# Kernel tuning notes

Hardware: AMD Instinct MI355X
Metric: run time of the kernel (lower is better)

## Reference

```python
import jax, jax.numpy as jnp
import numpy as np

VOCAB, EMB_DIM, HIDDEN, NUM_CLASSES = 50000, 300, 1000, 5
B, MAX_LEN = 4096, 128


def setup_inputs() -> dict:
    key = jax.random.key(0)
    k1, k2, k3, k4, k5, k6, k7 = jax.random.split(key, 7)
    x = jax.random.randint(k1, (B, MAX_LEN), 0, VOCAB, dtype=jnp.int64)
    lengths = jnp.maximum(jax.random.randint(k2, (B,), 0, MAX_LEN, dtype=jnp.int64), 1)
    emb_table = jax.random.normal(k3, (VOCAB, EMB_DIM), dtype=jnp.float32) * 0.1
    W1 = jax.random.normal(k4, (2 * EMB_DIM, HIDDEN), dtype=jnp.float32) * (1.0 / np.sqrt(2 * EMB_DIM))
    b1 = jax.random.normal(k5, (HIDDEN,), dtype=jnp.float32) * 0.01
    W2 = jax.random.normal(k6, (HIDDEN, NUM_CLASSES), dtype=jnp.float32) * (1.0 / np.sqrt(HIDDEN))
    b2 = jax.random.normal(k7, (NUM_CLASSES,), dtype=jnp.float32) * 0.01
    return {"x": x, "lengths": lengths, "emb_table": emb_table,
            "W1": W1, "b1": b1, "W2": W2, "b2": b2}


def reference(x, lengths, emb_table, W1, b1, W2, b2):
    emb = emb_table[x]                                  # [B, L, D] gather
    mask = (jnp.arange(emb.shape[1])[None, :] < lengths[:, None])  # [B, L]
    m = mask[:, :, None].astype(emb.dtype)
    avg_pool = jnp.sum(emb * m, axis=1) / lengths[:, None].astype(emb.dtype)  # [B, D]
    neg_inf = jnp.finfo(emb.dtype).min
    max_pool = jnp.max(jnp.where(mask[:, :, None], emb, neg_inf), axis=1)     # [B, D]
    rep = jnp.concatenate([avg_pool, max_pool], axis=1)  # [B, 2D]
    hidden = jax.nn.relu(rep @ W1 + b1)                  # [B, 1000]
    logits = hidden @ W2 + b2                            # [B, C]
    return logits
```

## Files before the change

### kernel.cpp

```cpp
#include <hip/hip_runtime.h>
#include <float.h>
#include <stdint.h>

#define EMB_DIM  300
#define MAX_LEN  128
#define HIDDEN   1000
#define NCLS     5
#define VOCAB_SZ 50000
#define KPAD     640
#define NPAD     1024
#define EMBPAD   320

typedef float    f32x4  __attribute__((ext_vector_type(4)));
typedef __bf16   bf16x8 __attribute__((ext_vector_type(8)));
typedef unsigned short ushort8v __attribute__((ext_vector_type(8)));

__device__ __forceinline__ unsigned short f2bf(float f) {
    union { float f; uint32_t u; } v; v.f = f;
    uint32_t u = v.u;
    return (unsigned short)((u + 0x7FFFu + ((u >> 16) & 1u)) >> 16);
}
__device__ __forceinline__ float bf2f(unsigned short h) {
    union { uint32_t u; float f; } v; v.u = ((uint32_t)h) << 16;
    return v.f;
}

__global__ __launch_bounds__(256) void convert_emb(
    const float* __restrict__ emb, unsigned short* __restrict__ embb)
{
    const int i = blockIdx.x * 256 + threadIdx.x;
    const int total = VOCAB_SZ * (EMBPAD / 4);
    if (i >= total) return;
    const int v  = i / (EMBPAD / 4);
    const int ch = i - v * (EMBPAD / 4);
    ushort4 o = {0, 0, 0, 0};
    if (ch < 75) {
        const float4 f = *(const float4*)(emb + (size_t)v * EMB_DIM + ch * 4);
        o.x = f2bf(f.x); o.y = f2bf(f.y); o.z = f2bf(f.z); o.w = f2bf(f.w);
    }
    *(ushort4*)(embb + (size_t)v * EMBPAD + ch * 4) = o;
}

__global__ __launch_bounds__(256) void transpose_w1(
    const float* __restrict__ W1, unsigned short* __restrict__ Bt)
{
    __shared__ float t[32][33];
    const int tx = threadIdx.x & 31, ty = threadIdx.x >> 5;
    const int n0 = blockIdx.x * 32, k0 = blockIdx.y * 32;
    #pragma unroll
    for (int i = 0; i < 4; ++i) {
        int k = k0 + ty + i * 8, n = n0 + tx;
        t[ty + i * 8][tx] = (k < 600 && n < HIDDEN) ? W1[(size_t)k * HIDDEN + n] : 0.f;
    }
    __syncthreads();
    #pragma unroll
    for (int i = 0; i < 4; ++i) {
        int n = n0 + ty + i * 8, k = k0 + tx;
        Bt[(size_t)n * KPAD + k] = f2bf(t[tx][ty + i * 8]);
    }
}

__global__ __launch_bounds__(256) void transpose_w2(
    const float* __restrict__ W2, unsigned short* __restrict__ W2t)
{
    const int i = blockIdx.x * 256 + threadIdx.x;
    if (i >= NCLS * 1024) return;
    const int c = i >> 10, k = i & 1023;
    const float v = (k < HIDDEN) ? W2[(size_t)k * NCLS + c] : 0.f;
    W2t[(size_t)c * 1024 + k] = f2bf(v);
}

__global__ __launch_bounds__(128) void pool_bf16(
    const int* __restrict__ x, const int* __restrict__ lengths,
    const unsigned short* __restrict__ embb, unsigned short* __restrict__ rep)
{
    const int b = blockIdx.x;
    const int t = threadIdx.x;

    __shared__ int sidx[MAX_LEN];
    sidx[t] = x[b * MAX_LEN + t];
    __syncthreads();

    unsigned short* rb = rep + (size_t)b * KPAD;

    if (t >= 75) {
        if (t < 85) {
            ushort4 z = {0, 0, 0, 0};
            *(ushort4*)(rb + 600 + (t - 75) * 4) = z;
        }
        return;
    }

    int L = lengths[b];
    L = max(1, min(L, MAX_LEN));

    const int d = t * 4;
    float4 s  = {0.f, 0.f, 0.f, 0.f};
    float4 mx = {-FLT_MAX, -FLT_MAX, -FLT_MAX, -FLT_MAX};

    int i = 0;
    for (; i + 2 <= L; i += 2) {
        int i0 = max(0, min(sidx[i],     VOCAB_SZ - 1));
        int i1 = max(0, min(sidx[i + 1], VOCAB_SZ - 1));
        const ushort4 a = *(const ushort4*)(embb + (size_t)i0 * EMBPAD + d);
        const ushort4 c = *(const ushort4*)(embb + (size_t)i1 * EMBPAD + d);
        float a0 = bf2f(a.x), a1 = bf2f(a.y), a2 = bf2f(a.z), a3 = bf2f(a.w);
        float c0 = bf2f(c.x), c1 = bf2f(c.y), c2 = bf2f(c.z), c3 = bf2f(c.w);
        s.x += a0 + c0; s.y += a1 + c1; s.z += a2 + c2; s.w += a3 + c3;
        mx.x = fmaxf(mx.x, fmaxf(a0, c0)); mx.y = fmaxf(mx.y, fmaxf(a1, c1));
        mx.z = fmaxf(mx.z, fmaxf(a2, c2)); mx.w = fmaxf(mx.w, fmaxf(a3, c3));
    }
    if (i < L) {
        int i0 = max(0, min(sidx[i], VOCAB_SZ - 1));
        const ushort4 a = *(const ushort4*)(embb + (size_t)i0 * EMBPAD + d);
        float a0 = bf2f(a.x), a1 = bf2f(a.y), a2 = bf2f(a.z), a3 = bf2f(a.w);
        s.x += a0; s.y += a1; s.z += a2; s.w += a3;
        mx.x = fmaxf(mx.x, a0); mx.y = fmaxf(mx.y, a1);
        mx.z = fmaxf(mx.z, a2); mx.w = fmaxf(mx.w, a3);
    }

    const float inv = 1.0f / (float)L;
    ushort4 av, mv;
    av.x = f2bf(s.x * inv); av.y = f2bf(s.y * inv);
    av.z = f2bf(s.z * inv); av.w = f2bf(s.w * inv);
    mv.x = f2bf(mx.x); mv.y = f2bf(mx.y); mv.z = f2bf(mx.z); mv.w = f2bf(mx.w);
    *(ushort4*)(rb + d)       = av;
    *(ushort4*)(rb + 300 + d) = mv;
}

__global__ __launch_bounds__(128) void pool_f32(
    const int* __restrict__ x, const int* __restrict__ lengths,
    const float* __restrict__ emb, unsigned short* __restrict__ rep)
{
    const int b = blockIdx.x;
    const int t = threadIdx.x;

    __shared__ int sidx[MAX_LEN];
    sidx[t] = x[b * MAX_LEN + t];
    __syncthreads();

    unsigned short* rb = rep + (size_t)b * KPAD;

    if (t >= 75) {
        if (t < 85) {
            ushort4 z = {0, 0, 0, 0};
            *(ushort4*)(rb + 600 + (t - 75) * 4) = z;
        }
        return;
    }

    int L = lengths[b];
    L = max(1, min(L, MAX_LEN));

    const int d = t * 4;
    float4 s  = {0.f, 0.f, 0.f, 0.f};
    float4 mx = {-FLT_MAX, -FLT_MAX, -FLT_MAX, -FLT_MAX};

    for (int i = 0; i < L; ++i) {
        int idx = max(0, min(sidx[i], VOCAB_SZ - 1));
        const float4 v = *(const float4*)(emb + (size_t)idx * EMB_DIM + d);
        s.x += v.x; s.y += v.y; s.z += v.z; s.w += v.w;
        mx.x = fmaxf(mx.x, v.x); mx.y = fmaxf(mx.y, v.y);
        mx.z = fmaxf(mx.z, v.z); mx.w = fmaxf(mx.w, v.w);
    }

    const float inv = 1.0f / (float)L;
    ushort4 av, mv;
    av.x = f2bf(s.x * inv); av.y = f2bf(s.y * inv);
    av.z = f2bf(s.z * inv); av.w = f2bf(s.w * inv);
    mv.x = f2bf(mx.x); mv.y = f2bf(mx.y); mv.z = f2bf(mx.z); mv.w = f2bf(mx.w);
    *(ushort4*)(rb + d)       = av;
    *(ushort4*)(rb + 300 + d) = mv;
}

#define BM 64
#define BN 64
#define BK 32

__global__ __launch_bounds__(256, 4) void gemm1_mfma(
    const unsigned short* __restrict__ A,
    const unsigned short* __restrict__ Bt,
    const float* __restrict__ bias,
    unsigned short* __restrict__ H,
    int M)
{
    __shared__ unsigned short As[2][BM * BK];
    __shared__ unsigned short Bs[2][BN * BK];

    const int tid  = threadIdx.x;
    const int wv   = tid >> 6;
    const int lane = tid & 63;
    const int bm   = blockIdx.y * BM;
    const int bn   = blockIdx.x * BN;
    const int wr   = (wv & 1) * 32;
    const int wc   = (wv >> 1) * 32;

    f32x4 acc[2][2] = {};

    auto stage = [&](int buf, int k0) {
        {
            int ci  = wv * 64 + lane;
            int row = ci >> 2, c = ci & 3;
            const unsigned short* g = A + (size_t)(bm + row) * KPAD + k0 + c * 8;
            unsigned short* l = &As[buf][wv * 512];
            __builtin_amdgcn_global_load_lds(g, l, 16, 0, 0);
        }
        {
            int ci  = wv * 64 + lane;
            int row = ci >> 2, c = ci & 3;
            const unsigned short* g = Bt + (size_t)(bn + row) * KPAD + k0 + c * 8;
            unsigned short* l = &Bs[buf][wv * 512];
            __builtin_amdgcn_global_load_lds(g, l, 16, 0, 0);
        }
    };

    stage(0, 0);
    int cur = 0;
    const int q = lane >> 4, r16 = lane & 15;

    #pragma unroll 1
    for (int it = 0; it < KPAD / BK; ++it) {
        __syncthreads();
        if (it + 1 < KPAD / BK) stage(cur ^ 1, (it + 1) * BK);

        bf16x8 af[2], bfr[2];
        #pragma unroll
        for (int mi = 0; mi < 2; ++mi)
            af[mi] = *(const bf16x8*)&As[cur][(wr + mi * 16 + r16) * BK + q * 8];
        #pragma unroll
        for (int nj = 0; nj < 2; ++nj)
            bfr[nj] = *(const bf16x8*)&Bs[cur][(wc + nj * 16 + r16) * BK + q * 8];
        #pragma unroll
        for (int mi = 0; mi < 2; ++mi)
            #pragma unroll
            for (int nj = 0; nj < 2; ++nj)
                acc[mi][nj] = __builtin_amdgcn_mfma_f32_16x16x32_bf16(
                    af[mi], bfr[nj], acc[mi][nj], 0, 0, 0);
        cur ^= 1;
    }

    #pragma unroll
    for (int nj = 0; nj < 2; ++nj) {
        int n = bn + wc + nj * 16 + r16;
        if (n >= HIDDEN) continue;
        float bv = bias[n];
        #pragma unroll
        for (int mi = 0; mi < 2; ++mi) {
            #pragma unroll
            for (int r = 0; r < 4; ++r) {
                int m = bm + wr + mi * 16 + q * 4 + r;
                float v = acc[mi][nj][r] + bv;
                H[(size_t)m * HIDDEN + n] = f2bf(fmaxf(v, 0.f));
            }
        }
    }
}

__global__ __launch_bounds__(256) void gemm2_kernel(
    const unsigned short* __restrict__ Hb,
    const unsigned short* __restrict__ W2t,
    const float* __restrict__ b2,
    float* __restrict__ out)
{
    const int wv   = threadIdx.x >> 6;
    const int lane = threadIdx.x & 63;
    const int b    = blockIdx.x * 4 + wv;
    const unsigned short* hr = Hb + (size_t)b * HIDDEN;

    float acc[NCLS] = {0.f, 0.f, 0.f, 0.f, 0.f};
    #pragma unroll
    for (int c = 0; c < 2; ++c) {
        int k0 = c * 512 + lane * 8;
        if (k0 + 8 <= HIDDEN) {
            ushort8v hv = *(const ushort8v*)(hr + k0);
            ushort8v wv8[NCLS];
            #pragma unroll
            for (int cc = 0; cc < NCLS; ++cc)
                wv8[cc] = *(const ushort8v*)(W2t + cc * 1024 + k0);
            #pragma unroll
            for (int j = 0; j < 8; ++j) {
                float h = bf2f(hv[j]);
                #pragma unroll
                for (int cc = 0; cc < NCLS; ++cc)
                    acc[cc] += h * bf2f(wv8[cc][j]);
            }
        }
    }
    #pragma unroll
    for (int off = 32; off > 0; off >>= 1)
        #pragma unroll
        for (int cc = 0; cc < NCLS; ++cc)
            acc[cc] += __shfl_down(acc[cc], off, 64);

    if (lane == 0) {
        #pragma unroll
        for (int cc = 0; cc < NCLS; ++cc)
            out[(size_t)b * NCLS + cc] = acc[cc] + b2[cc];
    }
}

extern "C" void kernel_launch(void* const* d_in, const int* in_sizes, int n_in,
                              void* d_out, int out_size, void* d_ws, size_t ws_size,
                              hipStream_t stream)
{
    const int*   x       = (const int*)d_in[0];
    const int*   lengths = (const int*)d_in[1];
    const float* emb     = (const float*)d_in[2];
    const float* W1      = (const float*)d_in[3];
    const float* b1      = (const float*)d_in[4];
    const float* W2      = (const float*)d_in[5];
    const float* b2      = (const float*)d_in[6];
    float*       out     = (float*)d_out;

    const int B = in_sizes[1];

    unsigned short* rep    = (unsigned short*)d_ws;
    unsigned short* w1t    = rep + (size_t)B * KPAD;
    unsigned short* w2t    = w1t + (size_t)NPAD * KPAD;
    unsigned short* hidden = w2t + (size_t)NCLS * 1024;
    unsigned short* embb   = hidden + (size_t)B * HIDDEN;

    const size_t need = ((size_t)B * KPAD + (size_t)NPAD * KPAD + NCLS * 1024
                         + (size_t)B * HIDDEN + (size_t)VOCAB_SZ * EMBPAD) * 2;

    transpose_w1<<<dim3(32, 20), 256, 0, stream>>>(W1, w1t);
    transpose_w2<<<(NCLS * 1024 + 255) / 256, 256, 0, stream>>>(W2, w2t);

    if (ws_size >= need) {
        const int total = VOCAB_SZ * (EMBPAD / 4);
        convert_emb<<<(total + 255) / 256, 256, 0, stream>>>(emb, embb);
        pool_bf16<<<B, 128, 0, stream>>>(x, lengths, embb, rep);
    } else {
        pool_f32<<<B, 128, 0, stream>>>(x, lengths, emb, rep);
    }

    dim3 g1(NPAD / BN, B / BM);
    gemm1_mfma<<<g1, 256, 0, stream>>>(rep, w1t, b1, hidden, B);

    gemm2_kernel<<<B / 4, 256, 0, stream>>>(hidden, w2t, b2, out);
}
```

Before: 161.3 us.

## Load GEMM1 MFMA fragments directly from global and merge weight prep kernels

The first GEMM no longer stages A and B tiles through double-buffered LDS with barriers. Each wave now loads its bf16x8 fragments straight from global memory (served mostly from L2) with a 4x unrolled K loop. The two weight-transpose kernels are also merged into one launch, with an extra grid column doing the W2 transpose. This drops LDS traffic and __syncthreads, at the cost of redundant global/L2 reads across waves and less latency hiding.

```diff
diff --git a/kernel.cpp b/kernel.cpp
--- a/kernel.cpp
+++ b/kernel.cpp
@@ -23,6 +23,33 @@
 __device__ __forceinline__ float bf2f(unsigned short h) {
     union { uint32_t u; float f; } v; v.u = ((uint32_t)h) << 16;
     return v.f;
+}
+
+__global__ __launch_bounds__(256) void prep_weights(
+    const float* __restrict__ W1, unsigned short* __restrict__ Bt,
+    const float* __restrict__ W2, unsigned short* __restrict__ W2t)
+{
+    if (blockIdx.x == 32) {
+        const int i = blockIdx.y * 256 + threadIdx.x;
+        const int c = i >> 10, k = i & 1023;
+        const float v = (k < HIDDEN) ? W2[(size_t)k * NCLS + c] : 0.f;
+        W2t[(size_t)c * 1024 + k] = f2bf(v);
+        return;
+    }
+    __shared__ float t[32][33];
+    const int tx = threadIdx.x & 31, ty = threadIdx.x >> 5;
+    const int n0 = blockIdx.x * 32, k0 = blockIdx.y * 32;
+    #pragma unroll
+    for (int i = 0; i < 4; ++i) {
+        int k = k0 + ty + i * 8, n = n0 + tx;
+        t[ty + i * 8][tx] = (k < 600 && n < HIDDEN) ? W1[(size_t)k * HIDDEN + n] : 0.f;
+    }
+    __syncthreads();
+    #pragma unroll
+    for (int i = 0; i < 4; ++i) {
+        int n = n0 + ty + i * 8, k = k0 + tx;
+        Bt[(size_t)n * KPAD + k] = f2bf(t[tx][ty + i * 8]);
+    }
 }
 
 __global__ __launch_bounds__(256) void convert_emb(
@@ -39,35 +66,6 @@
         o.x = f2bf(f.x); o.y = f2bf(f.y); o.z = f2bf(f.z); o.w = f2bf(f.w);
     }
     *(ushort4*)(embb + (size_t)v * EMBPAD + ch * 4) = o;
-}
-
-__global__ __launch_bounds__(256) void transpose_w1(
-    const float* __restrict__ W1, unsigned short* __restrict__ Bt)
-{
-    __shared__ float t[32][33];
-    const int tx = threadIdx.x & 31, ty = threadIdx.x >> 5;
-    const int n0 = blockIdx.x * 32, k0 = blockIdx.y * 32;
-    #pragma unroll
-    for (int i = 0; i < 4; ++i) {
-        int k = k0 + ty + i * 8, n = n0 + tx;
-        t[ty + i * 8][tx] = (k < 600 && n < HIDDEN) ? W1[(size_t)k * HIDDEN + n] : 0.f;
-    }
-    __syncthreads();
-    #pragma unroll
-    for (int i = 0; i < 4; ++i) {
-        int n = n0 + ty + i * 8, k = k0 + tx;
-        Bt[(size_t)n * KPAD + k] = f2bf(t[tx][ty + i * 8]);
-    }
-}
-
-__global__ __launch_bounds__(256) void transpose_w2(
-    const float* __restrict__ W2, unsigned short* __restrict__ W2t)
-{
-    const int i = blockIdx.x * 256 + threadIdx.x;
-    if (i >= NCLS * 1024) return;
-    const int c = i >> 10, k = i & 1023;
-    const float v = (k < HIDDEN) ? W2[(size_t)k * NCLS + c] : 0.f;
-    W2t[(size_t)c * 1024 + k] = f2bf(v);
 }
 
 __global__ __launch_bounds__(128) void pool_bf16(
@@ -173,82 +171,53 @@
     *(ushort4*)(rb + 300 + d) = mv;
 }
 
-#define BM 64
-#define BN 64
-#define BK 32
-
-__global__ __launch_bounds__(256, 4) void gemm1_mfma(
+#define GBM 64
+#define GBN 64
+
+__global__ __launch_bounds__(256, 4) void gemm1_flat(
     const unsigned short* __restrict__ A,
     const unsigned short* __restrict__ Bt,
     const float* __restrict__ bias,
     unsigned short* __restrict__ H,
     int M)
 {
-    __shared__ unsigned short As[2][BM * BK];
-    __shared__ unsigned short Bs[2][BN * BK];
-
     const int tid  = threadIdx.x;
     const int wv   = tid >> 6;
     const int lane = tid & 63;
-    const int bm   = blockIdx.y * BM;
-    const int bn   = blockIdx.x * BN;
-    const int wr   = (wv & 1) * 32;
-    const int wc   = (wv >> 1) * 32;
+    const int q    = lane >> 4, r16 = lane & 15;
+
+    const int bm = blockIdx.y * GBM + (wv & 1) * 32;
+    const int bn = blockIdx.x * GBN + (wv >> 1) * 32;
+
+    const unsigned short* a0 = A  + (size_t)(bm + r16) * KPAD + q * 8;
+    const unsigned short* a1 = a0 + (size_t)16 * KPAD;
+    const unsigned short* b0 = Bt + (size_t)(bn + r16) * KPAD + q * 8;
+    const unsigned short* b1 = b0 + (size_t)16 * KPAD;
 
     f32x4 acc[2][2] = {};
 
-    auto stage = [&](int buf, int k0) {
-        {
-            int ci  = wv * 64 + lane;
-            int row = ci >> 2, c = ci & 3;
-            const unsigned short* g = A + (size_t)(bm + row) * KPAD + k0 + c * 8;
-            unsigned short* l = &As[buf][wv * 512];
-            __builtin_amdgcn_global_load_lds(g, l, 16, 0, 0);
-        }
-        {
-            int ci  = wv * 64 + lane;
-            int row = ci >> 2, c = ci & 3;
-            const unsigned short* g = Bt + (size_t)(bn + row) * KPAD + k0 + c * 8;
-            unsigned short* l = &Bs[buf][wv * 512];
-            __builtin_amdgcn_global_load_lds(g, l, 16, 0, 0);
-        }
-    };
-
-    stage(0, 0);
-    int cur = 0;
-    const int q = lane >> 4, r16 = lane & 15;
-
-    #pragma unroll 1
-    for (int it = 0; it < KPAD / BK; ++it) {
-        __syncthreads();
-        if (it + 1 < KPAD / BK) stage(cur ^ 1, (it + 1) * BK);
-
-        bf16x8 af[2], bfr[2];
-        #pragma unroll
-        for (int mi = 0; mi < 2; ++mi)
-            af[mi] = *(const bf16x8*)&As[cur][(wr + mi * 16 + r16) * BK + q * 8];
-        #pragma unroll
-        for (int nj = 0; nj < 2; ++nj)
-            bfr[nj] = *(const bf16x8*)&Bs[cur][(wc + nj * 16 + r16) * BK + q * 8];
-        #pragma unroll
-        for (int mi = 0; mi < 2; ++mi)
-            #pragma unroll
-            for (int nj = 0; nj < 2; ++nj)
-                acc[mi][nj] = __builtin_amdgcn_mfma_f32_16x16x32_bf16(
-                    af[mi], bfr[nj], acc[mi][nj], 0, 0, 0);
-        cur ^= 1;
+    #pragma unroll 4
+    for (int k0 = 0; k0 < KPAD; k0 += 32) {
+        bf16x8 af0 = *(const bf16x8*)(a0 + k0);
+        bf16x8 af1 = *(const bf16x8*)(a1 + k0);
+        bf16x8 bf0 = *(const bf16x8*)(b0 + k0);
+        bf16x8 bf1 = *(const bf16x8*)(b1 + k0);
+        acc[0][0] = __builtin_amdgcn_mfma_f32_16x16x32_bf16(af0, bf0, acc[0][0], 0, 0, 0);
+        acc[0][1] = __builtin_amdgcn_mfma_f32_16x16x32_bf16(af0, bf1, acc[0][1], 0, 0, 0);
+        acc[1][0] = __builtin_amdgcn_mfma_f32_16x16x32_bf16(af1, bf0, acc[1][0], 0, 0, 0);
+        acc[1][1] = __builtin_amdgcn_mfma_f32_16x16x32_bf16(af1, bf1, acc[1][1], 0, 0, 0);
     }
 
     #pragma unroll
     for (int nj = 0; nj < 2; ++nj) {
-        int n = bn + wc + nj * 16 + r16;
+        int n = bn + nj * 16 + r16;
         if (n >= HIDDEN) continue;
         float bv = bias[n];
         #pragma unroll
         for (int mi = 0; mi < 2; ++mi) {
             #pragma unroll
             for (int r = 0; r < 4; ++r) {
-                int m = bm + wr + mi * 16 + q * 4 + r;
+                int m = bm + mi * 16 + q * 4 + r;
                 float v = acc[mi][nj][r] + bv;
                 H[(size_t)m * HIDDEN + n] = f2bf(fmaxf(v, 0.f));
             }
@@ -323,8 +292,7 @@
     const size_t need = ((size_t)B * KPAD + (size_t)NPAD * KPAD + NCLS * 1024
                          + (size_t)B * HIDDEN + (size_t)VOCAB_SZ * EMBPAD) * 2;
 
-    transpose_w1<<<dim3(32, 20), 256, 0, stream>>>(W1, w1t);
-    transpose_w2<<<(NCLS * 1024 + 255) / 256, 256, 0, stream>>>(W2, w2t);
+    prep_weights<<<dim3(33, 20), 256, 0, stream>>>(W1, w1t, W2, w2t);
 
     if (ws_size >= need) {
         const int total = VOCAB_SZ * (EMBPAD / 4);
@@ -334,8 +302,8 @@
         pool_f32<<<B, 128, 0, stream>>>(x, lengths, emb, rep);
     }
 
-    dim3 g1(NPAD / BN, B / BM);
-    gemm1_mfma<<<g1, 256, 0, stream>>>(rep, w1t, b1, hidden, B);
+    dim3 g1(NPAD / GBN, B / GBM);
+    gemm1_flat<<<g1, 256, 0, stream>>>(rep, w1t, b1, hidden, B);
 
     gemm2_kernel<<<B / 4, 256, 0, stream>>>(hidden, w2t, b2, out);
 }
```

Result: slower. 185.7 us (+15.2%).

## Fuse second GEMM into first GEMM epilogue and merge prep kernels

Applied to the files above, without the earlier changes.

The output projection is folded into gemm1's epilogue. Each block applies bias and ReLU, multiplies by its W2 slice, reduces across lanes and waves, and writes per-N-tile partial logits. A small reduce kernel then sums them with b2, so the bf16 hidden activation no longer has to be written and read back through global memory. The embedding conversion and both weight transposes now run in a single launch. The gemm1 K tile grows from 32 to 64 to halve the number of loop iterations and barriers. The cost is an extra partials buffer, one more reduce pass, and more LDS per block, which could lower occupancy.

```diff
diff --git a/kernel.cpp b/kernel.cpp
--- a/kernel.cpp
+++ b/kernel.cpp
@@ -15,6 +15,8 @@
 typedef __bf16   bf16x8 __attribute__((ext_vector_type(8)));
 typedef unsigned short ushort8v __attribute__((ext_vector_type(8)));
 
+#define CONV_BLOCKS ((VOCAB_SZ * (EMBPAD / 4) + 255) / 256)
+
 __device__ __forceinline__ unsigned short f2bf(float f) {
     union { float f; uint32_t u; } v; v.f = f;
     uint32_t u = v.u;
@@ -25,28 +27,38 @@
     return v.f;
 }
 
-__global__ __launch_bounds__(256) void convert_emb(
-    const float* __restrict__ emb, unsigned short* __restrict__ embb)
-{
-    const int i = blockIdx.x * 256 + threadIdx.x;
-    const int total = VOCAB_SZ * (EMBPAD / 4);
-    if (i >= total) return;
-    const int v  = i / (EMBPAD / 4);
-    const int ch = i - v * (EMBPAD / 4);
-    ushort4 o = {0, 0, 0, 0};
-    if (ch < 75) {
-        const float4 f = *(const float4*)(emb + (size_t)v * EMB_DIM + ch * 4);
-        o.x = f2bf(f.x); o.y = f2bf(f.y); o.z = f2bf(f.z); o.w = f2bf(f.w);
-    }
-    *(ushort4*)(embb + (size_t)v * EMBPAD + ch * 4) = o;
-}
-
-__global__ __launch_bounds__(256) void transpose_w1(
-    const float* __restrict__ W1, unsigned short* __restrict__ Bt)
+__global__ __launch_bounds__(256) void prep_all(
+    const float* __restrict__ emb, unsigned short* __restrict__ embb,
+    const float* __restrict__ W1, unsigned short* __restrict__ Bt,
+    const float* __restrict__ W2, unsigned short* __restrict__ W2t)
 {
     __shared__ float t[32][33];
+    const int blk = blockIdx.x;
+
+    if (blk < CONV_BLOCKS) {
+        const int i = blk * 256 + threadIdx.x;
+        if (i >= VOCAB_SZ * (EMBPAD / 4)) return;
+        const int v  = i / (EMBPAD / 4);
+        const int ch = i - v * (EMBPAD / 4);
+        ushort4 o = {0, 0, 0, 0};
+        if (ch < 75) {
+            const float4 f = *(const float4*)(emb + (size_t)v * EMB_DIM + ch * 4);
+            o.x = f2bf(f.x); o.y = f2bf(f.y); o.z = f2bf(f.z); o.w = f2bf(f.w);
+        }
+        *(ushort4*)(embb + (size_t)v * EMBPAD + ch * 4) = o;
+        return;
+    }
+    const int pb = blk - CONV_BLOCKS;
+    if (pb >= 640) {
+        const int i = (pb - 640) * 256 + threadIdx.x;
+        const int c = i >> 10, k = i & 1023;
+        const float v = (k < HIDDEN) ? W2[(size_t)k * NCLS + c] : 0.f;
+        W2t[(size_t)c * 1024 + k] = f2bf(v);
+        return;
+    }
+    const int px = pb & 31, py = pb >> 5;
     const int tx = threadIdx.x & 31, ty = threadIdx.x >> 5;
-    const int n0 = blockIdx.x * 32, k0 = blockIdx.y * 32;
+    const int n0 = px * 32, k0 = py * 32;
     #pragma unroll
     for (int i = 0; i < 4; ++i) {
         int k = k0 + ty + i * 8, n = n0 + tx;
@@ -58,16 +70,6 @@
         int n = n0 + ty + i * 8, k = k0 + tx;
         Bt[(size_t)n * KPAD + k] = f2bf(t[tx][ty + i * 8]);
     }
-}
-
-__global__ __launch_bounds__(256) void transpose_w2(
-    const float* __restrict__ W2, unsigned short* __restrict__ W2t)
-{
-    const int i = blockIdx.x * 256 + threadIdx.x;
-    if (i >= NCLS * 1024) return;
-    const int c = i >> 10, k = i & 1023;
-    const float v = (k < HIDDEN) ? W2[(size_t)k * NCLS + c] : 0.f;
-    W2t[(size_t)c * 1024 + k] = f2bf(v);
 }
 
 __global__ __launch_bounds__(128) void pool_bf16(
@@ -175,13 +177,14 @@
 
 #define BM 64
 #define BN 64
-#define BK 32
-
-__global__ __launch_bounds__(256, 4) void gemm1_mfma(
+#define BK 64
+
+__global__ __launch_bounds__(256, 4) void gemm1p(
     const unsigned short* __restrict__ A,
     const unsigned short* __restrict__ Bt,
     const float* __restrict__ bias,
-    unsigned short* __restrict__ H,
+    const unsigned short* __restrict__ W2t,
+    float* __restrict__ partials,
     int M)
 {
     __shared__ unsigned short As[2][BM * BK];
@@ -198,18 +201,20 @@
     f32x4 acc[2][2] = {};
 
     auto stage = [&](int buf, int k0) {
-        {
-            int ci  = wv * 64 + lane;
-            int row = ci >> 2, c = ci & 3;
+        #pragma unroll
+        for (int j = 0; j < 2; ++j) {
+            int ci  = (wv * 2 + j) * 64 + lane;
+            int row = ci >> 3, c = ci & 7;
             const unsigned short* g = A + (size_t)(bm + row) * KPAD + k0 + c * 8;
-            unsigned short* l = &As[buf][wv * 512];
+            unsigned short* l = &As[buf][(wv * 2 + j) * 512];
             __builtin_amdgcn_global_load_lds(g, l, 16, 0, 0);
         }
-        {
-            int ci  = wv * 64 + lane;
-            int row = ci >> 2, c = ci & 3;
+        #pragma unroll
+        for (int j = 0; j < 2; ++j) {
+            int ci  = (wv * 2 + j) * 64 + lane;
+            int row = ci >> 3, c = ci & 7;
             const unsigned short* g = Bt + (size_t)(bn + row) * KPAD + k0 + c * 8;
-            unsigned short* l = &Bs[buf][wv * 512];
+            unsigned short* l = &Bs[buf][(wv * 2 + j) * 512];
             __builtin_amdgcn_global_load_lds(g, l, 16, 0, 0);
         }
     };
@@ -223,80 +228,90 @@
         __syncthreads();
         if (it + 1 < KPAD / BK) stage(cur ^ 1, (it + 1) * BK);
 
-        bf16x8 af[2], bfr[2];
         #pragma unroll
-        for (int mi = 0; mi < 2; ++mi)
-            af[mi] = *(const bf16x8*)&As[cur][(wr + mi * 16 + r16) * BK + q * 8];
-        #pragma unroll
-        for (int nj = 0; nj < 2; ++nj)
-            bfr[nj] = *(const bf16x8*)&Bs[cur][(wc + nj * 16 + r16) * BK + q * 8];
-        #pragma unroll
-        for (int mi = 0; mi < 2; ++mi)
+        for (int ks = 0; ks < BK; ks += 32) {
+            bf16x8 af[2], bfr[2];
+            #pragma unroll
+            for (int mi = 0; mi < 2; ++mi)
+                af[mi] = *(const bf16x8*)&As[cur][(wr + mi * 16 + r16) * BK + ks + q * 8];
             #pragma unroll
             for (int nj = 0; nj < 2; ++nj)
-                acc[mi][nj] = __builtin_amdgcn_mfma_f32_16x16x32_bf16(
-                    af[mi], bfr[nj], acc[mi][nj], 0, 0, 0);
+                bfr[nj] = *(const bf16x8*)&Bs[cur][(wc + nj * 16 + r16) * BK + ks + q * 8];
+            #pragma unroll
+            for (int mi = 0; mi < 2; ++mi)
+                #pragma unroll
+                for (int nj = 0; nj < 2; ++nj)
+                    acc[mi][nj] = __builtin_amdgcn_mfma_f32_16x16x32_bf16(
+                        af[mi], bfr[nj], acc[mi][nj], 0, 0, 0);
+        }
         cur ^= 1;
     }
 
+    float bv[2], w2v[2][NCLS];
     #pragma unroll
     for (int nj = 0; nj < 2; ++nj) {
         int n = bn + wc + nj * 16 + r16;
-        if (n >= HIDDEN) continue;
-        float bv = bias[n];
+        if (n < HIDDEN) {
+            bv[nj] = bias[n];
+            #pragma unroll
+            for (int c = 0; c < NCLS; ++c) w2v[nj][c] = bf2f(W2t[c * 1024 + n]);
+        } else {
+            bv[nj] = 0.f;
+            #pragma unroll
+            for (int c = 0; c < NCLS; ++c) w2v[nj][c] = 0.f;
+        }
+    }
+
+    __syncthreads();
+    float* pl = (float*)As;
+
+    #pragma unroll
+    for (int mi = 0; mi < 2; ++mi) {
         #pragma unroll
-        for (int mi = 0; mi < 2; ++mi) {
-            #pragma unroll
-            for (int r = 0; r < 4; ++r) {
-                int m = bm + wr + mi * 16 + q * 4 + r;
-                float v = acc[mi][nj][r] + bv;
-                H[(size_t)m * HIDDEN + n] = f2bf(fmaxf(v, 0.f));
+        for (int r = 0; r < 4; ++r) {
+            float p[NCLS] = {0.f, 0.f, 0.f, 0.f, 0.f};
+            #pragma unroll
+            for (int nj = 0; nj < 2; ++nj) {
+                float h = fmaxf(acc[mi][nj][r] + bv[nj], 0.f);
+                #pragma unroll
+                for (int c = 0; c < NCLS; ++c) p[c] += h * w2v[nj][c];
             }
-        }
-    }
-}
-
-__global__ __launch_bounds__(256) void gemm2_kernel(
-    const unsigned short* __restrict__ Hb,
-    const unsigned short* __restrict__ W2t,
-    const float* __restrict__ b2,
-    float* __restrict__ out)
-{
-    const int wv   = threadIdx.x >> 6;
-    const int lane = threadIdx.x & 63;
-    const int b    = blockIdx.x * 4 + wv;
-    const unsigned short* hr = Hb + (size_t)b * HIDDEN;
-
-    float acc[NCLS] = {0.f, 0.f, 0.f, 0.f, 0.f};
-    #pragma unroll
-    for (int c = 0; c < 2; ++c) {
-        int k0 = c * 512 + lane * 8;
-        if (k0 + 8 <= HIDDEN) {
-            ushort8v hv = *(const ushort8v*)(hr + k0);
-            ushort8v wv8[NCLS];
-            #pragma unroll
-            for (int cc = 0; cc < NCLS; ++cc)
-                wv8[cc] = *(const ushort8v*)(W2t + cc * 1024 + k0);
-            #pragma unroll
-            for (int j = 0; j < 8; ++j) {
-                float h = bf2f(hv[j]);
+            #pragma unroll
+            for (int off = 1; off < 16; off <<= 1)
                 #pragma unroll
-                for (int cc = 0; cc < NCLS; ++cc)
-                    acc[cc] += h * bf2f(wv8[cc][j]);
+                for (int c = 0; c < NCLS; ++c)
+                    p[c] += __shfl_xor(p[c], off, 64);
+            if (r16 == 0) {
+                int lr = mi * 16 + q * 4 + r;
+                #pragma unroll
+                for (int c = 0; c < NCLS; ++c)
+                    pl[(wv * 32 + lr) * NCLS + c] = p[c];
             }
         }
     }
-    #pragma unroll
-    for (int off = 32; off > 0; off >>= 1)
-        #pragma unroll
-        for (int cc = 0; cc < NCLS; ++cc)
-            acc[cc] += __shfl_down(acc[cc], off, 64);
-
-    if (lane == 0) {
-        #pragma unroll
-        for (int cc = 0; cc < NCLS; ++cc)
-            out[(size_t)b * NCLS + cc] = acc[cc] + b2[cc];
-    }
+    __syncthreads();
+
+    for (int e = tid; e < BM * NCLS; e += 256) {
+        int lr = e / NCLS, c = e - lr * NCLS;
+        float v;
+        if (lr < 32) v = pl[(0 * 32 + lr) * NCLS + c] + pl[(2 * 32 + lr) * NCLS + c];
+        else         v = pl[(1 * 32 + lr - 32) * NCLS + c] + pl[(3 * 32 + lr - 32) * NCLS + c];
+        partials[(size_t)blockIdx.x * M * NCLS + (size_t)(bm + lr) * NCLS + c] = v;
+    }
+}
+
+__global__ __launch_bounds__(256) void reduce_out(
+    const float* __restrict__ partials, const float* __restrict__ b2,
+    float* __restrict__ out, int M)
+{
+    const int i = blockIdx.x * 256 + threadIdx.x;
+    if (i >= M * NCLS) return;
+    const int c = i % NCLS;
+    float s = b2[c];
+    #pragma unroll
+    for (int nb = 0; nb < NPAD / BN; ++nb)
+        s += partials[(size_t)nb * M * NCLS + i];
+    out[i] = s;
 }
 
 extern "C" void kernel_launch(void* const* d_in, const int* in_sizes, int n_in,
@@ -314,28 +329,26 @@
 
     const int B = in_sizes[1];
 
-    unsigned short* rep    = (unsigned short*)d_ws;
-    unsigned short* w1t    = rep + (size_t)B * KPAD;
-    unsigned short* w2t    = w1t + (size_t)NPAD * KPAD;
-    unsigned short* hidden = w2t + (size_t)NCLS * 1024;
-    unsigned short* embb   = hidden + (size_t)B * HIDDEN;
+    unsigned short* rep      = (unsigned short*)d_ws;
+    unsigned short* w1t      = rep + (size_t)B * KPAD;
+    unsigned short* w2t      = w1t + (size_t)NPAD * KPAD;
+    unsigned short* embb     = w2t + (size_t)NCLS * 1024;
+    float*          partials = (float*)(embb + (size_t)VOCAB_SZ * EMBPAD);
 
     const size_t need = ((size_t)B * KPAD + (size_t)NPAD * KPAD + NCLS * 1024
-                         + (size_t)B * HIDDEN + (size_t)VOCAB_SZ * EMBPAD) * 2;
-
-    transpose_w1<<<dim3(32, 20), 256, 0, stream>>>(W1, w1t);
-    transpose_w2<<<(NCLS * 1024 + 255) / 256, 256, 0, stream>>>(W2, w2t);
+                         + (size_t)VOCAB_SZ * EMBPAD) * 2
+                        + (size_t)(NPAD / BN) * B * NCLS * 4;
+
+    prep_all<<<CONV_BLOCKS + 660, 256, 0, stream>>>(emb, embb, W1, w1t, W2, w2t);
 
     if (ws_size >= need) {
-        const int total = VOCAB_SZ * (EMBPAD / 4);
-        convert_emb<<<(total + 255) / 256, 256, 0, stream>>>(emb, embb);
         pool_bf16<<<B, 128, 0, stream>>>(x, lengths, embb, rep);
     } else {
         pool_f32<<<B, 128, 0, stream>>>(x, lengths, emb, rep);
     }
 
     dim3 g1(NPAD / BN, B / BM);
-    gemm1_mfma<<<g1, 256, 0, stream>>>(rep, w1t, b1, hidden, B);
-
-    gemm2_kernel<<<B / 4, 256, 0, stream>>>(hidden, w2t, b2, out);
-}
+    gemm1p<<<g1, 256, 0, stream>>>(rep, w1t, b1, w2t, partials, B);
+
+    reduce_out<<<(B * NCLS + 255) / 256, 256, 0, stream>>>(partials, b2, out, B);
+}
```

Result: no change. 160.4 us (-0.6%).
